# Optimization experiments

Hardware: AMD Instinct MI355X
Metric: run time of the kernel (lower is better)

Reference implementation:

```python
import jax, jax.numpy as jnp
import numpy as np

N = 1_000_000      # number of samples
C = 100            # number of classes
N_BINS = 20        # adaptive-ECE bins (equal-count)
TEMPERATURE = 1.0


def setup_inputs() -> dict:
    key = jax.random.key(0)
    k1, k2 = jax.random.split(key)
    logits = jax.random.normal(k1, (N, C), dtype=jnp.float32)
    labels = jax.random.randint(k2, (N,), 0, C)
    return {"logits": logits, "labels": labels}


def reference(logits, labels):
    # softmax with temperature, top-1 confidence + prediction
    softmaxes = jax.nn.softmax(logits / TEMPERATURE, axis=1)
    confidences = jnp.max(softmaxes, axis=1)            # [N]
    predictions = jnp.argmax(softmaxes, axis=1)         # [N]
    accuracies = (predictions == labels).astype(confidences.dtype)  # [N]

    # sort by confidence ascending; carry accuracies along
    order = jnp.argsort(confidences)
    conf_sorted = confidences[order]
    acc_sorted = accuracies[order]

    num = logits.shape[0]
    window = num // N_BINS            # samples per adaptive bin
    n_full = num // window            # number of flushed bins (== N_BINS when divisible)
    m = n_full * window

    # equal-count binning == reshape + mean (replaces the per-sample python loop)
    conf_bins = conf_sorted[:m].reshape(n_full, window).mean(axis=1)  # avg conf / bin
    acc_bins = acc_sorted[:m].reshape(n_full, window).mean(axis=1)    # accuracy / bin

    ece = jnp.sum(jnp.abs(conf_bins - acc_bins)) * (window / num)
    return jnp.reshape(ece, (1,)), acc_bins
```

## Files before the change

### kernel.cpp

```cpp
#include <hip/hip_runtime.h>
#include <stdint.h>

typedef uint32_t u32;
typedef uint64_t u64;
typedef uint8_t  u8;

#define KEY_MIN   0x3C000000u
#define SUBSHIFT  10
#define NBUCK     57344
#define NBINS     20
#define NB        19

__device__ __forceinline__ u32 bucket_of(u32 key) {
    if (key < KEY_MIN) return 0u;
    u32 b = (key - KEY_MIN) >> SUBSHIFT;
    return b < (u32)NBUCK ? b : (u32)(NBUCK - 1);
}

__global__ __launch_bounds__(256) void k1_conf100(
        const float* __restrict__ logits, const int* __restrict__ labels,
        u32* __restrict__ keys, u8* __restrict__ accb, u32* __restrict__ hist,
        int N) {
    const int C4 = 25;
    int lane = threadIdx.x & 63;
    int wid  = (blockIdx.x * (blockDim.x >> 6)) + (threadIdx.x >> 6);
    int g    = lane >> 4;
    int sub  = lane & 15;
    int r    = wid * 4 + g;
    if (r >= N) return;

    const float4* row4 = (const float4*)(logits + (size_t)r * 100);
    float4 v0 = row4[sub];
    float4 v1;
    bool has2 = (sub + 16) < C4;
    if (has2) v1 = row4[sub + 16];
    else      v1 = make_float4(-3.4e38f, -3.4e38f, -3.4e38f, -3.4e38f);

    float m = v0.x; int am = 4 * sub;
    if (v0.y > m) { m = v0.y; am = 4 * sub + 1; }
    if (v0.z > m) { m = v0.z; am = 4 * sub + 2; }
    if (v0.w > m) { m = v0.w; am = 4 * sub + 3; }
    int b2 = 64 + 4 * sub;
    if (v1.x > m) { m = v1.x; am = b2; }
    if (v1.y > m) { m = v1.y; am = b2 + 1; }
    if (v1.z > m) { m = v1.z; am = b2 + 2; }
    if (v1.w > m) { m = v1.w; am = b2 + 3; }

    #pragma unroll
    for (int off = 8; off >= 1; off >>= 1) {
        float om = __shfl_xor(m, off);
        int   oa = __shfl_xor(am, off);
        if (om > m || (om == m && oa < am)) { m = om; am = oa; }
    }

    float s = __expf(v0.x - m) + __expf(v0.y - m) + __expf(v0.z - m) + __expf(v0.w - m);
    if (has2) s += __expf(v1.x - m) + __expf(v1.y - m) + __expf(v1.z - m) + __expf(v1.w - m);
    #pragma unroll
    for (int off = 8; off >= 1; off >>= 1) s += __shfl_xor(s, off);

    if (sub == 0) {
        float conf = 1.0f / s;
        u32 key = __float_as_uint(conf);
        keys[r] = key;
        accb[r] = (labels[r] == am) ? (u8)1 : (u8)0;
        atomicAdd(&hist[bucket_of(key)], 1u);
    }
}

__global__ __launch_bounds__(256) void k1_generic(
        const float* __restrict__ logits, const int* __restrict__ labels,
        u32* __restrict__ keys, u8* __restrict__ accb, u32* __restrict__ hist,
        int N, int C) {
    int i = blockIdx.x * blockDim.x + threadIdx.x;
    if (i >= N) return;
    const float* row = logits + (size_t)i * (size_t)C;
    float m = -3.4e38f, s = 0.f;
    int am = 0;
    for (int c = 0; c < C; c++) {
        float v = row[c];
        float nm = fmaxf(m, v); am = (v > m) ? c : am;
        s = s * __expf(m - nm) + __expf(v - nm); m = nm;
    }
    float conf = 1.0f / s;
    u32 key = __float_as_uint(conf);
    keys[i] = key;
    accb[i] = (labels[i] == am) ? (u8)1 : (u8)0;
    atomicAdd(&hist[bucket_of(key)], 1u);
}

__global__ void k2_scan(const u32* __restrict__ hist, u32* __restrict__ meta,
                        u32 W) {
    __shared__ u32 sp[1024];
    int t = threadIdx.x;
    const int PER = NBUCK / 1024;
    u32 s = 0;
    for (int k = 0; k < PER; k++) s += hist[t * PER + k];
    sp[t] = s; __syncthreads();
    for (int d = 1; d < 1024; d <<= 1) {
        u32 v = (t >= d) ? sp[t - d] : 0u;
        __syncthreads();
        sp[t] += v;
        __syncthreads();
    }
    u32 cum = sp[t] - s;
    for (int k = 0; k < PER; k++) {
        u32 c = hist[t * PER + k];
        if (c) {
            for (int j = 0; j < NB; j++) {
                u32 r = (u32)(j + 1) * W;
                if (cum < r && r <= cum + c) {
                    meta[j] = (u32)(t * PER + k);
                    meta[NB + j] = r - cum;
                }
            }
        }
        cum += c;
    }
}

__global__ __launch_bounds__(256) void k3_subhist(
        const u32* __restrict__ keys, const u32* __restrict__ meta,
        u32* __restrict__ subhist, int N) {
    __shared__ u32 sB[NB];
    if (threadIdx.x < NB) sB[threadIdx.x] = meta[threadIdx.x];
    __syncthreads();
    int total4 = N >> 2;
    const uint4* k4 = (const uint4*)keys;
    for (int i = blockIdx.x * blockDim.x + threadIdx.x; i < total4;
         i += gridDim.x * blockDim.x) {
        uint4 kv = k4[i];
        u32 ks[4] = {kv.x, kv.y, kv.z, kv.w};
        #pragma unroll
        for (int e = 0; e < 4; e++) {
            u32 b = bucket_of(ks[e]);
            #pragma unroll
            for (int j = 0; j < NB; j++)
                if (b == sB[j]) atomicAdd(&subhist[j * 1024 + (ks[e] & 1023u)], 1u);
        }
    }
    for (int i = (total4 << 2) + blockIdx.x * blockDim.x + threadIdx.x; i < N;
         i += gridDim.x * blockDim.x) {
        u32 k = keys[i];
        u32 b = bucket_of(k);
        for (int j = 0; j < NB; j++)
            if (b == sB[j]) atomicAdd(&subhist[j * 1024 + (k & 1023u)], 1u);
    }
}

__global__ void k4_resolve(const u32* __restrict__ subhist, u32* __restrict__ meta) {
    int j = blockIdx.x;
    int t = threadIdx.x;
    __shared__ u32 sh[256];
    u32 v[4];
    #pragma unroll
    for (int k = 0; k < 4; k++) v[k] = subhist[j * 1024 + t * 4 + k];
    u32 tsum = v[0] + v[1] + v[2] + v[3];
    sh[t] = tsum; __syncthreads();
    for (int d = 1; d < 256; d <<= 1) {
        u32 x = (t >= d) ? sh[t - d] : 0u;
        __syncthreads(); sh[t] += x; __syncthreads();
    }
    u32 run = sh[t] - tsum;
    u32 off = meta[NB + j];
    u32 bkt = meta[j];
    #pragma unroll
    for (int k = 0; k < 4; k++) {
        if (run < off && off <= run + v[k])
            meta[2 * NB + j] = KEY_MIN + (bkt << SUBSHIFT) + (u32)(t * 4 + k);
        run += v[k];
    }
}

__global__ __launch_bounds__(256) void k7_accum(
        const u32* __restrict__ keys, const u8* __restrict__ accb,
        const u32* __restrict__ meta, u64* __restrict__ confQ,
        u32* __restrict__ accCnt, int N) {
    __shared__ unsigned long long lc[4][NBINS];
    __shared__ u32 la[4][NBINS];
    __shared__ u32 sK[NB];
    int t = threadIdx.x;
    int w = t >> 6;
    if (t < 4 * NBINS) { lc[t / NBINS][t % NBINS] = 0ull; la[t / NBINS][t % NBINS] = 0u; }
    if (t < NB) sK[t] = meta[2 * NB + t];
    __syncthreads();
    int total4 = N >> 2;
    const uint4*  k4 = (const uint4*)keys;
    const uchar4* a4 = (const uchar4*)accb;
    for (int i = blockIdx.x * blockDim.x + t; i < total4; i += gridDim.x * blockDim.x) {
        uint4  kv = k4[i];
        uchar4 av = a4[i];
        u32 ks[4] = {kv.x, kv.y, kv.z, kv.w};
        u32 as[4] = {av.x, av.y, av.z, av.w};
        #pragma unroll
        for (int e = 0; e < 4; e++) {
            int bin = 0;
            #pragma unroll
            for (int j = 0; j < NB; j++) bin += (ks[e] > sK[j]) ? 1 : 0;
            float conf = __uint_as_float(ks[e]);
            u64 q = (u64)(conf * 4294967296.0f);
            atomicAdd(&lc[w][bin], (unsigned long long)q);
            atomicAdd(&la[w][bin], as[e]);
        }
    }
    for (int i = (total4 << 2) + blockIdx.x * blockDim.x + t; i < N;
         i += gridDim.x * blockDim.x) {
        u32 k = keys[i];
        int bin = 0;
        for (int j = 0; j < NB; j++) bin += (k > sK[j]) ? 1 : 0;
        u64 q = (u64)(__uint_as_float(k) * 4294967296.0f);
        atomicAdd(&lc[w][bin], (unsigned long long)q);
        atomicAdd(&la[w][bin], (u32)accb[i]);
    }
    __syncthreads();
    if (t < NBINS) {
        unsigned long long cq = lc[0][t] + lc[1][t] + lc[2][t] + lc[3][t];
        u32 ac = la[0][t] + la[1][t] + la[2][t] + la[3][t];
        if (cq) atomicAdd((unsigned long long*)&confQ[t], cq);
        if (ac) atomicAdd(&accCnt[t], ac);
    }
}

__global__ void k8_final(const u64* __restrict__ confQ, const u32* __restrict__ accCnt,
                         float* __restrict__ out, int W, int N) {
    if (threadIdx.x == 0 && blockIdx.x == 0) {
        double ece = 0.0;
        for (int b = 0; b < NBINS; b++) {
            double cm = (double)confQ[b] * (1.0 / 4294967296.0) / (double)W;
            double am = (double)accCnt[b] / (double)W;
            ece += fabs(cm - am);
            out[1 + b] = (float)am;
        }
        out[0] = (float)(ece * (double)W / (double)N);
    }
}

extern "C" void kernel_launch(void* const* d_in, const int* in_sizes, int n_in,
                              void* d_out, int out_size, void* d_ws, size_t ws_size,
                              hipStream_t stream) {
    const float* logits = (const float*)d_in[0];
    const int*   labels = (const int*)d_in[1];
    int N = in_sizes[1];
    int C = in_sizes[0] / N;
    float* out = (float*)d_out;

    u8* ws = (u8*)d_ws;
    u32* keys = (u32*)ws;
    u8*  accb = ws + (size_t)4 * N;
    size_t aux = ((size_t)5 * N + 255) & ~(size_t)255;
    u64* confQ   = (u64*)(ws + aux);
    u32* accCnt  = (u32*)(ws + aux + 160);
    u32* hist    = (u32*)(ws + aux + 256);
    u32* subhist = (u32*)(ws + aux + 229632);
    u32* meta    = (u32*)(ws + aux + 307456);
    size_t zbytes = 307456 + 228;

    hipMemsetAsync(ws + aux, 0, zbytes, stream);

    u32 W = (u32)(N / NBINS);

    if (C == 100) {
        int blocks1 = (N + 15) / 16;
        k1_conf100<<<blocks1, 256, 0, stream>>>(logits, labels, keys, accb, hist, N);
    } else {
        int blocks1 = (N + 255) / 256;
        k1_generic<<<blocks1, 256, 0, stream>>>(logits, labels, keys, accb, hist, N, C);
    }
    k2_scan   <<<1, 1024, 0, stream>>>(hist, meta, W);
    k3_subhist<<<1024, 256, 0, stream>>>(keys, meta, subhist, N);
    k4_resolve<<<NB, 256, 0, stream>>>(subhist, meta);
    k7_accum  <<<1024, 256, 0, stream>>>(keys, accb, meta, confQ, accCnt, N);
    k8_final  <<<1, 64, 0, stream>>>(confQ, accCnt, out, (int)W, N);
}
```

Baseline: 190.5 us.

## Merge sub-histogram pass into accumulation by sorting boundary-bucket samples in one block

Removes the separate sub-histogram and resolve kernels that made an extra full pass over the keys. The accumulation kernel now bins samples by coarse bucket and appends samples from boundary buckets to a small global list. A single-block final kernel bitonic-sorts that list in shared memory, finds the exact boundary keys, and adds those samples to the correct bins. The list is capped at a fixed capacity, so results become wrong if boundary buckets hold more samples than the cap, and the single-block sort adds serial tail work.

```diff
diff --git a/kernel.cpp b/kernel.cpp
--- a/kernel.cpp
+++ b/kernel.cpp
@@ -10,6 +10,7 @@
 #define NBUCK     57344
 #define NBINS     20
 #define NB        19
+#define LISTCAP   2048
 
 __device__ __forceinline__ u32 bucket_of(u32 key) {
     if (key < KEY_MIN) return 0u;
@@ -118,70 +119,18 @@
     }
 }
 
-__global__ __launch_bounds__(256) void k3_subhist(
-        const u32* __restrict__ keys, const u32* __restrict__ meta,
-        u32* __restrict__ subhist, int N) {
-    __shared__ u32 sB[NB];
-    if (threadIdx.x < NB) sB[threadIdx.x] = meta[threadIdx.x];
-    __syncthreads();
-    int total4 = N >> 2;
-    const uint4* k4 = (const uint4*)keys;
-    for (int i = blockIdx.x * blockDim.x + threadIdx.x; i < total4;
-         i += gridDim.x * blockDim.x) {
-        uint4 kv = k4[i];
-        u32 ks[4] = {kv.x, kv.y, kv.z, kv.w};
-        #pragma unroll
-        for (int e = 0; e < 4; e++) {
-            u32 b = bucket_of(ks[e]);
-            #pragma unroll
-            for (int j = 0; j < NB; j++)
-                if (b == sB[j]) atomicAdd(&subhist[j * 1024 + (ks[e] & 1023u)], 1u);
-        }
-    }
-    for (int i = (total4 << 2) + blockIdx.x * blockDim.x + threadIdx.x; i < N;
-         i += gridDim.x * blockDim.x) {
-        u32 k = keys[i];
-        u32 b = bucket_of(k);
-        for (int j = 0; j < NB; j++)
-            if (b == sB[j]) atomicAdd(&subhist[j * 1024 + (k & 1023u)], 1u);
-    }
-}
-
-__global__ void k4_resolve(const u32* __restrict__ subhist, u32* __restrict__ meta) {
-    int j = blockIdx.x;
-    int t = threadIdx.x;
-    __shared__ u32 sh[256];
-    u32 v[4];
-    #pragma unroll
-    for (int k = 0; k < 4; k++) v[k] = subhist[j * 1024 + t * 4 + k];
-    u32 tsum = v[0] + v[1] + v[2] + v[3];
-    sh[t] = tsum; __syncthreads();
-    for (int d = 1; d < 256; d <<= 1) {
-        u32 x = (t >= d) ? sh[t - d] : 0u;
-        __syncthreads(); sh[t] += x; __syncthreads();
-    }
-    u32 run = sh[t] - tsum;
-    u32 off = meta[NB + j];
-    u32 bkt = meta[j];
-    #pragma unroll
-    for (int k = 0; k < 4; k++) {
-        if (run < off && off <= run + v[k])
-            meta[2 * NB + j] = KEY_MIN + (bkt << SUBSHIFT) + (u32)(t * 4 + k);
-        run += v[k];
-    }
-}
-
-__global__ __launch_bounds__(256) void k7_accum(
+__global__ __launch_bounds__(256) void k37_accum(
         const u32* __restrict__ keys, const u8* __restrict__ accb,
         const u32* __restrict__ meta, u64* __restrict__ confQ,
-        u32* __restrict__ accCnt, int N) {
+        u32* __restrict__ accCnt, u64* __restrict__ list, u32* __restrict__ listCnt,
+        int N) {
     __shared__ unsigned long long lc[4][NBINS];
     __shared__ u32 la[4][NBINS];
-    __shared__ u32 sK[NB];
+    __shared__ u32 sB[NB];
     int t = threadIdx.x;
     int w = t >> 6;
     if (t < 4 * NBINS) { lc[t / NBINS][t % NBINS] = 0ull; la[t / NBINS][t % NBINS] = 0u; }
-    if (t < NB) sK[t] = meta[2 * NB + t];
+    if (t < NB) sB[t] = meta[t];
     __syncthreads();
     int total4 = N >> 2;
     const uint4*  k4 = (const uint4*)keys;
@@ -193,23 +142,38 @@
         u32 as[4] = {av.x, av.y, av.z, av.w};
         #pragma unroll
         for (int e = 0; e < 4; e++) {
-            int bin = 0;
+            u32 b = bucket_of(ks[e]);
+            int bin = 0; bool isB = false;
             #pragma unroll
-            for (int j = 0; j < NB; j++) bin += (ks[e] > sK[j]) ? 1 : 0;
-            float conf = __uint_as_float(ks[e]);
-            u64 q = (u64)(conf * 4294967296.0f);
-            atomicAdd(&lc[w][bin], (unsigned long long)q);
-            atomicAdd(&la[w][bin], as[e]);
+            for (int j = 0; j < NB; j++) {
+                bin += (b > sB[j]) ? 1 : 0;
+                isB |= (b == sB[j]);
+            }
+            if (isB) {
+                u32 p = atomicAdd(listCnt, 1u);
+                if (p < (u32)LISTCAP) list[p] = ((u64)ks[e] << 1) | (u64)as[e];
+            } else {
+                u64 q = (u64)(__uint_as_float(ks[e]) * 4294967296.0f);
+                atomicAdd(&lc[w][bin], (unsigned long long)q);
+                atomicAdd(&la[w][bin], as[e]);
+            }
         }
     }
     for (int i = (total4 << 2) + blockIdx.x * blockDim.x + t; i < N;
          i += gridDim.x * blockDim.x) {
         u32 k = keys[i];
-        int bin = 0;
-        for (int j = 0; j < NB; j++) bin += (k > sK[j]) ? 1 : 0;
-        u64 q = (u64)(__uint_as_float(k) * 4294967296.0f);
-        atomicAdd(&lc[w][bin], (unsigned long long)q);
-        atomicAdd(&la[w][bin], (u32)accb[i]);
+        u32 ac = (u32)accb[i];
+        u32 b = bucket_of(k);
+        int bin = 0; bool isB = false;
+        for (int j = 0; j < NB; j++) { bin += (b > sB[j]) ? 1 : 0; isB |= (b == sB[j]); }
+        if (isB) {
+            u32 p = atomicAdd(listCnt, 1u);
+            if (p < (u32)LISTCAP) list[p] = ((u64)k << 1) | (u64)ac;
+        } else {
+            u64 q = (u64)(__uint_as_float(k) * 4294967296.0f);
+            atomicAdd(&lc[w][bin], (unsigned long long)q);
+            atomicAdd(&la[w][bin], ac);
+        }
     }
     __syncthreads();
     if (t < NBINS) {
@@ -220,13 +184,69 @@
     }
 }
 
-__global__ void k8_final(const u64* __restrict__ confQ, const u32* __restrict__ accCnt,
-                         float* __restrict__ out, int W, int N) {
-    if (threadIdx.x == 0 && blockIdx.x == 0) {
+__global__ __launch_bounds__(256) void k48_final(
+        const u64* __restrict__ list, const u32* __restrict__ listCnt,
+        const u32* __restrict__ meta, const u64* __restrict__ confQ,
+        const u32* __restrict__ accCnt, float* __restrict__ out, u32 W, int N) {
+    __shared__ u64 S[LISTCAP];
+    __shared__ u32 sB[NB], sOff[NB], sKj[NB];
+    __shared__ unsigned long long bc[NBINS];
+    __shared__ u32 ba[NBINS];
+    int t = threadIdx.x;
+    u32 cnt = *listCnt; if (cnt > (u32)LISTCAP) cnt = LISTCAP;
+    for (int i = t; i < LISTCAP; i += 256) S[i] = (i < (int)cnt) ? list[i] : ~0ull;
+    if (t < NB) { sB[t] = meta[t]; sOff[t] = meta[NB + t]; }
+    if (t < NBINS) { bc[t] = 0ull; ba[t] = 0u; }
+    __syncthreads();
+
+    for (int k = 2; k <= LISTCAP; k <<= 1) {
+        for (int j = k >> 1; j > 0; j >>= 1) {
+            for (int i = t; i < LISTCAP; i += 256) {
+                int ix = i ^ j;
+                if (ix > i) {
+                    u64 a = S[i], b = S[ix];
+                    bool up = ((i & k) == 0);
+                    if ((a > b) == up) { S[i] = b; S[ix] = a; }
+                }
+            }
+            __syncthreads();
+        }
+    }
+
+    if (t < NB) {
+        u32 lo = 0, hi = cnt;
+        while (lo < hi) {
+            u32 mid = (lo + hi) >> 1;
+            u32 kk = (u32)(S[mid] >> 1);
+            if (bucket_of(kk) < sB[t]) lo = mid + 1; else hi = mid;
+        }
+        u32 pos = lo + sOff[t] - 1;
+        if (pos >= cnt) pos = cnt ? cnt - 1 : 0;
+        sKj[t] = (u32)(S[pos] >> 1);
+    }
+    __syncthreads();
+
+    for (int i = t; i < (int)cnt; i += 256) {
+        u32 kk = (u32)(S[i] >> 1);
+        u32 ac = (u32)(S[i] & 1ull);
+        u32 b = bucket_of(kk);
+        int bin = 0;
+        #pragma unroll
+        for (int j = 0; j < NB; j++)
+            bin += ((b > sB[j]) || (b == sB[j] && kk > sKj[j])) ? 1 : 0;
+        u64 q = (u64)(__uint_as_float(kk) * 4294967296.0f);
+        atomicAdd(&bc[bin], (unsigned long long)q);
+        atomicAdd(&ba[bin], ac);
+    }
+    __syncthreads();
+
+    if (t == 0) {
         double ece = 0.0;
         for (int b = 0; b < NBINS; b++) {
-            double cm = (double)confQ[b] * (1.0 / 4294967296.0) / (double)W;
-            double am = (double)accCnt[b] / (double)W;
+            u64 cq = confQ[b] + (u64)bc[b];
+            u32 ac = accCnt[b] + ba[b];
+            double cm = (double)cq * (1.0 / 4294967296.0) / (double)W;
+            double am = (double)ac / (double)W;
             ece += fabs(cm - am);
             out[1 + b] = (float)am;
         }
@@ -249,10 +269,12 @@
     size_t aux = ((size_t)5 * N + 255) & ~(size_t)255;
     u64* confQ   = (u64*)(ws + aux);
     u32* accCnt  = (u32*)(ws + aux + 160);
+    u32* listCnt = (u32*)(ws + aux + 240);
     u32* hist    = (u32*)(ws + aux + 256);
-    u32* subhist = (u32*)(ws + aux + 229632);
-    u32* meta    = (u32*)(ws + aux + 307456);
-    size_t zbytes = 307456 + 228;
+    u32* meta    = (u32*)(ws + aux + 229632);
+    size_t zbytes = 229784;
+    size_t loff = (aux + zbytes + 255) & ~(size_t)255;
+    u64* list    = (u64*)(ws + loff);
 
     hipMemsetAsync(ws + aux, 0, zbytes, stream);
 
@@ -265,9 +287,7 @@
         int blocks1 = (N + 255) / 256;
         k1_generic<<<blocks1, 256, 0, stream>>>(logits, labels, keys, accb, hist, N, C);
     }
-    k2_scan   <<<1, 1024, 0, stream>>>(hist, meta, W);
-    k3_subhist<<<1024, 256, 0, stream>>>(keys, meta, subhist, N);
-    k4_resolve<<<NB, 256, 0, stream>>>(subhist, meta);
-    k7_accum  <<<1024, 256, 0, stream>>>(keys, accb, meta, confQ, accCnt, N);
-    k8_final  <<<1, 64, 0, stream>>>(confQ, accCnt, out, (int)W, N);
-}
+    k2_scan  <<<1, 1024, 0, stream>>>(hist, meta, W);
+    k37_accum<<<512, 256, 0, stream>>>(keys, accb, meta, confQ, accCnt, list, listCnt, N);
+    k48_final<<<1, 256, 0, stream>>>(list, listCnt, meta, confQ, accCnt, out, W, N);
+}
```

Result: slower. 247.5 us (+30.0%).
